# Kernel optimization log

Measured on AMD Instinct MI355X. Metric: run time of the kernel, lower is better.

## Reference

```python
import jax, jax.numpy as jnp
import numpy as np
from jax import lax

D_MODEL = 1024
D_STATE = 16
D_CONV = 4
EXPAND = 2
D_INNER = EXPAND * D_MODEL            # 2048
DT_RANK = (D_MODEL + 15) // 16        # 64
B, L = 2, 2048
EPS = 1e-5


def setup_inputs() -> dict:
    key = jax.random.key(0)
    ks = jax.random.split(key, 12)
    s = 0.02
    x = jax.random.normal(ks[0], (B, L, D_MODEL), dtype=jnp.float32)
    norm_w = jnp.ones((D_MODEL,), dtype=jnp.float32)
    in_proj_w = jax.random.normal(ks[1], (2 * D_INNER, D_MODEL), dtype=jnp.float32) * s
    conv_w = jax.random.normal(ks[2], (D_INNER, D_CONV), dtype=jnp.float32) * 0.1
    conv_b = jax.random.normal(ks[3], (D_INNER,), dtype=jnp.float32) * 0.01
    x_proj_w = jax.random.normal(ks[4], (DT_RANK + 2 * D_STATE, D_INNER), dtype=jnp.float32) * s
    dt_proj_w = jax.random.normal(ks[5], (D_INNER, DT_RANK), dtype=jnp.float32) * 0.1
    dt_proj_b = jax.random.normal(ks[6], (D_INNER,), dtype=jnp.float32) * 0.5 - 4.0  # small softplus(delta)
    # S4D-real init: A = -(1..d_state) per channel
    A_log = jnp.log(jnp.broadcast_to(jnp.arange(1, D_STATE + 1, dtype=jnp.float32), (D_INNER, D_STATE)))
    Dp = jnp.ones((D_INNER,), dtype=jnp.float32)
    out_proj_w = jax.random.normal(ks[7], (D_MODEL, D_INNER), dtype=jnp.float32) * s
    return {"x": x, "norm_w": norm_w, "in_proj_w": in_proj_w, "conv_w": conv_w,
            "conv_b": conv_b, "x_proj_w": x_proj_w, "dt_proj_w": dt_proj_w,
            "dt_proj_b": dt_proj_b, "A_log": A_log, "Dp": Dp, "out_proj_w": out_proj_w}


def _selective_scan(deltaA, deltaBu, Cm):
    # deltaA, deltaBu: [B,L,Di,N]; Cm: [B,L,N] -> y: [B,L,Di]
    def step(h, inp):
        dA, dBu, c = inp
        h = dA * h + dBu                       # [B,Di,N]
        y = jnp.einsum('bdn,bn->bd', h, c)     # [B,Di]
        return h, y
    h0 = jnp.zeros(deltaA.shape[0:1] + deltaA.shape[2:], deltaA.dtype)
    _, ys = lax.scan(step, h0, (deltaA.transpose(1, 0, 2, 3),
                                deltaBu.transpose(1, 0, 2, 3),
                                Cm.transpose(1, 0, 2)))
    return ys.transpose(1, 0, 2)               # [B,L,Di]


def reference(x, norm_w, in_proj_w, conv_w, conv_b, x_proj_w,
              dt_proj_w, dt_proj_b, A_log, Dp, out_proj_w):
    d_inner, d_conv = conv_w.shape
    d_state = A_log.shape[1]
    dt_rank = dt_proj_w.shape[1]

    # RMSNorm
    rms = jnp.sqrt(jnp.mean(x * x, axis=-1, keepdims=True) + EPS)
    xn = norm_w * (x / rms)

    # input projection -> x, z streams
    xz = jnp.einsum('bld,ed->ble', xn, in_proj_w)      # [B,L,2*Di]
    xi, z = jnp.split(xz, 2, axis=-1)

    # depthwise causal conv1d + SiLU
    xc = lax.conv_general_dilated(
        xi.transpose(0, 2, 1), conv_w[:, None, :], (1,), [(d_conv - 1, 0)],
        dimension_numbers=('NCL', 'OIL', 'NCL'), feature_group_count=d_inner)
    xc = jax.nn.silu(xc.transpose(0, 2, 1) + conv_b)   # [B,L,Di]

    # input-dependent SSM params
    dbl = jnp.einsum('bld,ed->ble', xc, x_proj_w)      # [B,L,dt_rank+2N]
    dt, Bm, Cm = jnp.split(dbl, [dt_rank, dt_rank + d_state], axis=-1)
    delta = jax.nn.softplus(jnp.einsum('blr,dr->bld', dt, dt_proj_w) + dt_proj_b)

    A = -jnp.exp(A_log)                                # [Di,N]
    deltaA = jnp.exp(delta[..., None] * A)             # [B,L,Di,N]
    deltaBu = delta[..., None] * Bm[:, :, None, :] * xc[..., None]

    y = _selective_scan(deltaA, deltaBu, Cm)           # [B,L,Di]
    y = y + xc * Dp
    y = y * jax.nn.silu(z)

    out = jnp.einsum('bld,ed->ble', y, out_proj_w)     # [B,L,d_model]
    return x + out
```

## Files before the change

kernel.cpp:

```cpp
#include <hip/hip_runtime.h>
#include <hip/hip_bf16.h>
#include <math.h>

#define D_MODEL 1024
#define D_STATE 16
#define D_CONV 4
#define D_INNER 2048
#define DT_RANK 64
#define BATCH 2
#define SEQ 2048
#define NTOK (BATCH*SEQ)
#define EPS 1e-5f
#define CCH 32
#define TCH (SEQ/CCH)
#define XKS 8
#define XKC (D_INNER/XKS)

typedef __attribute__((ext_vector_type(8))) short short8;
typedef __attribute__((ext_vector_type(4))) float f32x4;
typedef __attribute__((ext_vector_type(4))) unsigned short us4;

__device__ inline unsigned short f2bf(float f) {
  union { __hip_bfloat16 h; unsigned short u; } c;
  c.h = __float2bfloat16(f);
  return c.u;
}

#define GLL(gp, lp) __builtin_amdgcn_global_load_lds( \
    (const __attribute__((address_space(1))) void*)(gp), \
    (__attribute__((address_space(3))) void*)(lp), 16, 0, 0)

__global__ __launch_bounds__(256) void f2bf_kernel(const float* __restrict__ in,
                                                   unsigned short* __restrict__ out, int n) {
  int i = (blockIdx.x * 256 + threadIdx.x) * 4;
  if (i >= n) return;
  float4 v = *(const float4*)(in + i);
  us4 o;
  o[0] = f2bf(v.x); o[1] = f2bf(v.y); o[2] = f2bf(v.z); o[3] = f2bf(v.w);
  *(us4*)(out + i) = o;
}

__global__ __launch_bounds__(256) void rmsnorm_kernel(const float* __restrict__ x,
                                                      const float* __restrict__ w,
                                                      unsigned short* __restrict__ xn) {
  int tok = blockIdx.x;
  const float* xr = x + (size_t)tok * D_MODEL;
  unsigned short* xo = xn + (size_t)tok * D_MODEL;
  int t = threadIdx.x;
  float4 v = ((const float4*)xr)[t];
  float ss = v.x*v.x + v.y*v.y + v.z*v.z + v.w*v.w;
  #pragma unroll
  for (int off = 32; off > 0; off >>= 1) ss += __shfl_down(ss, off, 64);
  __shared__ float wsum[4];
  __shared__ float rinv_s;
  int lane = t & 63, wv = t >> 6;
  if (lane == 0) wsum[wv] = ss;
  __syncthreads();
  if (t == 0) {
    float tot = wsum[0] + wsum[1] + wsum[2] + wsum[3];
    rinv_s = 1.0f / sqrtf(tot / (float)D_MODEL + EPS);
  }
  __syncthreads();
  float rinv = rinv_s;
  float4 g = ((const float4*)w)[t];
  us4 o;
  o[0] = f2bf(v.x * rinv * g.x);
  o[1] = f2bf(v.y * rinv * g.y);
  o[2] = f2bf(v.z * rinv * g.z);
  o[3] = f2bf(v.w * rinv * g.w);
  *(us4*)(xo + t*4) = o;
}

template<int EPI>
__global__ __launch_bounds__(256) void gemm_bf16_kernel(
    const unsigned short* __restrict__ A,
    const unsigned short* __restrict__ W,
    float* __restrict__ C, int ldc, int K,
    const float* __restrict__ bias,
    const float* __restrict__ resid)
{
  __shared__ __align__(16) unsigned short Abuf[8*64*8];
  __shared__ __align__(16) unsigned short Bbuf[8*64*8];
  int tid = threadIdx.x;
  int lane = tid & 63;
  int w = tid >> 6;
  int bm = blockIdx.x * 128;
  int bn = blockIdx.y * 128;
  int wrow = (w >> 1) * 64;
  int wcol = (w & 1) * 64;

  int r15 = lane & 15, g = lane >> 4;
  const unsigned short* Ag0 = A + (size_t)(bm + 2*w*16 + r15) * K + g*8;
  const unsigned short* Ag1 = Ag0 + (size_t)16 * K;
  const unsigned short* Wg0 = W + (size_t)(bn + 2*w*16 + r15) * K + g*8;
  const unsigned short* Wg1 = Wg0 + (size_t)16 * K;
  unsigned short* Al0 = &Abuf[(2*w  )*512];
  unsigned short* Al1 = &Abuf[(2*w+1)*512];
  unsigned short* Bl0 = &Bbuf[(2*w  )*512];
  unsigned short* Bl1 = &Bbuf[(2*w+1)*512];

  f32x4 acc[4][4] = {};

  for (int k0 = 0; k0 < K; k0 += 32) {
    __syncthreads();
    GLL(Ag0 + k0, Al0);
    GLL(Ag1 + k0, Al1);
    GLL(Wg0 + k0, Bl0);
    GLL(Wg1 + k0, Bl1);
    __syncthreads();

    short8 af[4], bfr[4];
    #pragma unroll
    for (int i = 0; i < 4; ++i)
      af[i] = *(const short8*)&Abuf[((wrow >> 4) + i)*512 + lane*8];
    #pragma unroll
    for (int j = 0; j < 4; ++j)
      bfr[j] = *(const short8*)&Bbuf[((wcol >> 4) + j)*512 + lane*8];
    #pragma unroll
    for (int i = 0; i < 4; ++i)
      #pragma unroll
      for (int j = 0; j < 4; ++j)
        acc[i][j] = __builtin_amdgcn_mfma_f32_16x16x32_bf16(af[i], bfr[j], acc[i][j], 0, 0, 0);
  }

  #pragma unroll
  for (int i = 0; i < 4; ++i) {
    #pragma unroll
    for (int j = 0; j < 4; ++j) {
      #pragma unroll
      for (int r = 0; r < 4; ++r) {
        int row = bm + wrow + i*16 + (lane >> 4)*4 + r;
        int col = bn + wcol + j*16 + (lane & 15);
        float v = acc[i][j][r];
        if (EPI == 1) {
          float s = v + bias[col];
          v = fmaxf(s, 0.f) + log1pf(__expf(-fabsf(s)));
        } else if (EPI == 2) {
          v += resid[(size_t)row * ldc + col];
        }
        C[(size_t)row * ldc + col] = v;
      }
    }
  }
}

__global__ __launch_bounds__(256) void xproj_bf16_kernel(
    const unsigned short* __restrict__ A,
    const unsigned short* __restrict__ W,
    float* __restrict__ Ppart)
{
  __shared__ __align__(16) unsigned short Abuf[8*512];
  __shared__ __align__(16) unsigned short Bbuf[6*512];
  int tid = threadIdx.x;
  int lane = tid & 63;
  int w = tid >> 6;
  int bm = blockIdx.x * 128;
  int kc = blockIdx.y;
  const int K = D_INNER;
  int r15 = lane & 15, g = lane >> 4;

  const unsigned short* Ag0 = A + (size_t)(bm + 2*w*16 + r15) * K + g*8 + kc*XKC;
  const unsigned short* Ag1 = Ag0 + (size_t)16 * K;
  const unsigned short* Wg0 = W + (size_t)(w*16 + r15) * K + g*8 + kc*XKC;
  const unsigned short* Wg1 = W + (size_t)((4+w)*16 + r15) * K + g*8 + kc*XKC;
  unsigned short* Al0 = &Abuf[(2*w  )*512];
  unsigned short* Al1 = &Abuf[(2*w+1)*512];
  unsigned short* Bl0 = &Bbuf[w*512];
  unsigned short* Bl1 = &Bbuf[(4+w)*512];

  f32x4 acc[2][6] = {};

  for (int k0 = 0; k0 < XKC; k0 += 32) {
    __syncthreads();
    GLL(Ag0 + k0, Al0);
    GLL(Ag1 + k0, Al1);
    GLL(Wg0 + k0, Bl0);
    if (w < 2) GLL(Wg1 + k0, Bl1);
    __syncthreads();

    short8 af[2], bfr[6];
    #pragma unroll
    for (int i = 0; i < 2; ++i)
      af[i] = *(const short8*)&Abuf[(2*w + i)*512 + lane*8];
    #pragma unroll
    for (int j = 0; j < 6; ++j)
      bfr[j] = *(const short8*)&Bbuf[j*512 + lane*8];
    #pragma unroll
    for (int i = 0; i < 2; ++i)
      #pragma unroll
      for (int j = 0; j < 6; ++j)
        acc[i][j] = __builtin_amdgcn_mfma_f32_16x16x32_bf16(af[i], bfr[j], acc[i][j], 0, 0, 0);
  }

  float* out = Ppart + (size_t)kc * NTOK * 96;
  #pragma unroll
  for (int i = 0; i < 2; ++i) {
    #pragma unroll
    for (int j = 0; j < 6; ++j) {
      #pragma unroll
      for (int r = 0; r < 4; ++r) {
        int row = bm + w*32 + i*16 + (lane >> 4)*4 + r;
        int col = j*16 + (lane & 15);
        out[(size_t)row * 96 + col] = acc[i][j][r];
      }
    }
  }
}

__global__ __launch_bounds__(256) void xproj_reduce_kernel(
    const float* __restrict__ Ppart, float* __restrict__ dbl,
    unsigned short* __restrict__ dtbf)
{
  int idx = blockIdx.x * 256 + threadIdx.x;
  float s = 0.f;
  #pragma unroll
  for (int k = 0; k < XKS; ++k) s += Ppart[(size_t)k * NTOK * 96 + idx];
  dbl[idx] = s;
  int row = idx / 96, col = idx - row * 96;
  if (col < DT_RANK) dtbf[(size_t)row * DT_RANK + col] = f2bf(s);
}

__global__ __launch_bounds__(256) void conv_silu_kernel(
    const float* __restrict__ xz, const float* __restrict__ cw,
    const float* __restrict__ cb, float* __restrict__ xc,
    unsigned short* __restrict__ xcbf)
{
  int idx = blockIdx.x * 256 + threadIdx.x;
  int d = idx & (D_INNER - 1);
  int tok = idx >> 11;
  int l = tok & (SEQ - 1);
  float w0 = cw[d*4+0], w1 = cw[d*4+1], w2 = cw[d*4+2], w3 = cw[d*4+3];
  const float* xi = xz + (size_t)tok * (2*D_INNER) + d;
  float s = cb[d];
  s += (l >= 3 ? xi[-3*(2*D_INNER)] : 0.f) * w0;
  s += (l >= 2 ? xi[-2*(2*D_INNER)] : 0.f) * w1;
  s += (l >= 1 ? xi[-1*(2*D_INNER)] : 0.f) * w2;
  s += xi[0] * w3;
  float v = s / (1.f + __expf(-s));
  xc[idx] = v;
  xcbf[idx] = f2bf(v);
}

__global__ __launch_bounds__(256) void scan_pass1(
    const float* __restrict__ delta, const float* __restrict__ dbl,
    const float* __restrict__ xc, const float* __restrict__ A_log,
    float* __restrict__ P, float* __restrict__ He)
{
  int blk = blockIdx.x;
  int d = (blk & 7) * 256 + threadIdx.x;
  int c = (blk >> 3) & (CCH - 1);
  int b = blk >> 8;
  float Adn[16];
  #pragma unroll
  for (int n = 0; n < 16; ++n) Adn[n] = -__expf(A_log[d*16 + n]);
  float h[16] = {};
  float sdl = 0.f;
  int tok0 = b * SEQ + c * TCH;
  for (int t = 0; t < TCH; ++t) {
    size_t tok = (size_t)(tok0 + t);
    float dl = delta[tok * D_INNER + d];
    float xcv = xc[tok * D_INNER + d];
    float u = dl * xcv;
    const float4* bp = (const float4*)(dbl + tok*96 + 64);
    float4 b0 = bp[0], b1 = bp[1], b2 = bp[2], b3 = bp[3];
    float bv[16] = {b0.x,b0.y,b0.z,b0.w, b1.x,b1.y,b1.z,b1.w,
                    b2.x,b2.y,b2.z,b2.w, b3.x,b3.y,b3.z,b3.w};
    sdl += dl;
    #pragma unroll
    for (int n = 0; n < 16; ++n)
      h[n] = fmaf(__expf(dl * Adn[n]), h[n], u * bv[n]);
  }
  size_t base = ((size_t)(b*CCH + c) * 16) * D_INNER + d;
  #pragma unroll
  for (int n = 0; n < 16; ++n) {
    P [base + (size_t)n * D_INNER] = __expf(Adn[n] * sdl);
    He[base + (size_t)n * D_INNER] = h[n];
  }
}

__global__ __launch_bounds__(256) void scan_pass2(
    const float* __restrict__ P, const float* __restrict__ He,
    float* __restrict__ Hin)
{
  int blk = blockIdx.x;
  int d = (blk & 7) * 256 + threadIdx.x;
  int n = (blk >> 3) & 15;
  int b = blk >> 7;
  float h = 0.f;
  #pragma unroll 4
  for (int c = 0; c < CCH; ++c) {
    size_t idx = ((size_t)(b*CCH + c) * 16 + n) * D_INNER + d;
    Hin[idx] = h;
    h = fmaf(P[idx], h, He[idx]);
  }
}

__global__ __launch_bounds__(256) void scan_pass3(
    const float* __restrict__ delta, const float* __restrict__ dbl,
    const float* __restrict__ xc, const float* __restrict__ xz,
    const float* __restrict__ A_log, const float* __restrict__ Dp,
    const float* __restrict__ Hin, unsigned short* __restrict__ y)
{
  int blk = blockIdx.x;
  int d = (blk & 7) * 256 + threadIdx.x;
  int c = (blk >> 3) & (CCH - 1);
  int b = blk >> 8;
  float Adn[16];
  #pragma unroll
  for (int n = 0; n < 16; ++n) Adn[n] = -__expf(A_log[d*16 + n]);
  float Dpd = Dp[d];
  float h[16];
  size_t base = ((size_t)(b*CCH + c) * 16) * D_INNER + d;
  #pragma unroll
  for (int n = 0; n < 16; ++n) h[n] = Hin[base + (size_t)n * D_INNER];
  int tok0 = b * SEQ + c * TCH;
  for (int t = 0; t < TCH; ++t) {
    size_t tok = (size_t)(tok0 + t);
    float dl = delta[tok * D_INNER + d];
    float xcv = xc[tok * D_INNER + d];
    float u = dl * xcv;
    const float4* bp = (const float4*)(dbl + tok*96 + 64);
    float4 b0 = bp[0], b1 = bp[1], b2 = bp[2], b3 = bp[3];
    float4 c0 = bp[4], c1 = bp[5], c2 = bp[6], c3 = bp[7];
    float bv[16] = {b0.x,b0.y,b0.z,b0.w, b1.x,b1.y,b1.z,b1.w,
                    b2.x,b2.y,b2.z,b2.w, b3.x,b3.y,b3.z,b3.w};
    float cv[16] = {c0.x,c0.y,c0.z,c0.w, c1.x,c1.y,c1.z,c1.w,
                    c2.x,c2.y,c2.z,c2.w, c3.x,c3.y,c3.z,c3.w};
    float z = xz[tok * (2*D_INNER) + D_INNER + d];
    float acc = xcv * Dpd;
    #pragma unroll
    for (int n = 0; n < 16; ++n) {
      h[n] = fmaf(__expf(dl * Adn[n]), h[n], u * bv[n]);
      acc = fmaf(h[n], cv[n], acc);
    }
    float sz = z / (1.f + __expf(-z));
    y[tok * D_INNER + d] = f2bf(acc * sz);
  }
}

extern "C" void kernel_launch(void* const* d_in, const int* in_sizes, int n_in,
                              void* d_out, int out_size, void* d_ws, size_t ws_size,
                              hipStream_t stream) {
  const float* x         = (const float*)d_in[0];
  const float* norm_w    = (const float*)d_in[1];
  const float* in_proj_w = (const float*)d_in[2];
  const float* conv_w    = (const float*)d_in[3];
  const float* conv_b    = (const float*)d_in[4];
  const float* x_proj_w  = (const float*)d_in[5];
  const float* dt_proj_w = (const float*)d_in[6];
  const float* dt_proj_b = (const float*)d_in[7];
  const float* A_log     = (const float*)d_in[8];
  const float* Dp        = (const float*)d_in[9];
  const float* out_proj_w= (const float*)d_in[10];
  float* out = (float*)d_out;

  char* ws = (char*)d_ws;
  float*          xz      = (float*)(ws);
  float*          xc      = (float*)(ws + ( 64ull<<20));
  float*          dbl     = (float*)(ws + ( 96ull<<20));
  float*          delta   = (float*)(ws + ( 98ull<<20));
  unsigned short* xcbf    = (unsigned short*)(ws + ( 98ull<<20));
  unsigned short* xn_bf   = (unsigned short*)(ws + (130ull<<20));
  unsigned short* w_in_bf = (unsigned short*)(ws + (138ull<<20));
  float*          Ppart   = (float*)(ws + (130ull<<20));
  unsigned short* dtbf    = (unsigned short*)(ws + (144ull<<20));
  unsigned short* w_out_bf= (unsigned short*)(ws + (146ull<<20));
  unsigned short* yb_bf   = (unsigned short*)(ws + (150ull<<20));
  float*          Pst     = (float*)(ws + (130ull<<20));
  float*          Hest    = (float*)(ws + (138ull<<20));
  float*          Hin     = (float*)(ws + (166ull<<20));
  unsigned short* w_xp_bf = (unsigned short*)(ws + (166ull<<20));
  unsigned short* w_dt_bf = (unsigned short*)(ws + (167ull<<20));

  rmsnorm_kernel<<<NTOK, 256, 0, stream>>>(x, norm_w, xn_bf);

  f2bf_kernel<<<(2*D_INNER*D_MODEL)/1024, 256, 0, stream>>>(in_proj_w, w_in_bf, 2*D_INNER*D_MODEL);
  f2bf_kernel<<<(D_MODEL*D_INNER)/1024, 256, 0, stream>>>(out_proj_w, w_out_bf, D_MODEL*D_INNER);
  f2bf_kernel<<<(96*D_INNER)/1024, 256, 0, stream>>>(x_proj_w, w_xp_bf, 96*D_INNER);
  f2bf_kernel<<<(D_INNER*DT_RANK)/1024, 256, 0, stream>>>(dt_proj_w, w_dt_bf, D_INNER*DT_RANK);

  {
    dim3 g(NTOK/128, (2*D_INNER)/128);
    gemm_bf16_kernel<0><<<g, 256, 0, stream>>>(xn_bf, w_in_bf, xz, 2*D_INNER, D_MODEL,
                                               nullptr, nullptr);
  }

  conv_silu_kernel<<<(NTOK*D_INNER)/256, 256, 0, stream>>>(xz, conv_w, conv_b, xc, xcbf);

  {
    dim3 g(NTOK/128, XKS);
    xproj_bf16_kernel<<<g, 256, 0, stream>>>(xcbf, w_xp_bf, Ppart);
    xproj_reduce_kernel<<<(NTOK*96)/256, 256, 0, stream>>>(Ppart, dbl, dtbf);
  }

  {
    dim3 g(NTOK/128, D_INNER/128);
    gemm_bf16_kernel<1><<<g, 256, 0, stream>>>(dtbf, w_dt_bf, delta, D_INNER, DT_RANK,
                                               dt_proj_b, nullptr);
  }

  scan_pass1<<<BATCH*CCH*8, 256, 0, stream>>>(delta, dbl, xc, A_log, Pst, Hest);
  scan_pass2<<<BATCH*16*8, 256, 0, stream>>>(Pst, Hest, Hin);
  scan_pass3<<<BATCH*CCH*8, 256, 0, stream>>>(delta, dbl, xc, xz, A_log, Dp, Hin, yb_bf);

  {
    dim3 g(NTOK/128, D_MODEL/128);
    gemm_bf16_kernel<2><<<g, 256, 0, stream>>>(yb_bf, w_out_bf, out, D_MODEL, D_INNER,
                                               nullptr, x);
  }
}
```

Baseline: 390.0 us.

## Store intermediate activations in bf16 and merge weight conversion launches

The in_proj GEMM now writes xz in bf16 and the dt_proj GEMM writes delta in bf16. The conv kernel reads bf16 four channels at a time and writes only a bf16 xc, and the scan passes read these bf16 buffers. This roughly halves the memory traffic for the large intermediates, drops the fp32 xc copy, and folds the four weight-conversion launches into one. The trade-off is lower precision for delta, xc and z going into the recurrent scan, which could push results past the tolerance.

```diff
diff --git a/kernel.cpp b/kernel.cpp
--- a/kernel.cpp
+++ b/kernel.cpp
@@ -25,15 +25,29 @@
   c.h = __float2bfloat16(f);
   return c.u;
 }
+__device__ inline float bf2f(unsigned short u) {
+  union { unsigned int i; float f; } c;
+  c.i = ((unsigned int)u) << 16;
+  return c.f;
+}
 
 #define GLL(gp, lp) __builtin_amdgcn_global_load_lds( \
     (const __attribute__((address_space(1))) void*)(gp), \
     (__attribute__((address_space(3))) void*)(lp), 16, 0, 0)
 
-__global__ __launch_bounds__(256) void f2bf_kernel(const float* __restrict__ in,
-                                                   unsigned short* __restrict__ out, int n) {
-  int i = (blockIdx.x * 256 + threadIdx.x) * 4;
-  if (i >= n) return;
+__global__ __launch_bounds__(256) void f2bf4_kernel(
+    const float* __restrict__ i0, unsigned short* __restrict__ o0, int b0,
+    const float* __restrict__ i1, unsigned short* __restrict__ o1, int b1,
+    const float* __restrict__ i2, unsigned short* __restrict__ o2, int b2,
+    const float* __restrict__ i3, unsigned short* __restrict__ o3)
+{
+  int blk = blockIdx.x;
+  const float* in; unsigned short* out; int base;
+  if (blk < b0)           { in = i0; out = o0; base = blk; }
+  else if (blk < b0+b1)   { in = i1; out = o1; base = blk - b0; }
+  else if (blk < b0+b1+b2){ in = i2; out = o2; base = blk - b0 - b1; }
+  else                    { in = i3; out = o3; base = blk - b0 - b1 - b2; }
+  int i = (base*256 + threadIdx.x)*4;
   float4 v = *(const float4*)(in + i);
   us4 o;
   o[0] = f2bf(v.x); o[1] = f2bf(v.y); o[2] = f2bf(v.z); o[3] = f2bf(v.w);
@@ -71,11 +85,11 @@
   *(us4*)(xo + t*4) = o;
 }
 
-template<int EPI>
+template<int EPI, int OBF>
 __global__ __launch_bounds__(256) void gemm_bf16_kernel(
     const unsigned short* __restrict__ A,
     const unsigned short* __restrict__ W,
-    float* __restrict__ C, int ldc, int K,
+    void* __restrict__ Cv, int ldc, int K,
     const float* __restrict__ bias,
     const float* __restrict__ resid)
 {
@@ -138,7 +152,8 @@
         } else if (EPI == 2) {
           v += resid[(size_t)row * ldc + col];
         }
-        C[(size_t)row * ldc + col] = v;
+        if (OBF) ((unsigned short*)Cv)[(size_t)row * ldc + col] = f2bf(v);
+        else     ((float*)Cv)[(size_t)row * ldc + col] = v;
       }
     }
   }
@@ -221,29 +236,39 @@
 }
 
 __global__ __launch_bounds__(256) void conv_silu_kernel(
-    const float* __restrict__ xz, const float* __restrict__ cw,
-    const float* __restrict__ cb, float* __restrict__ xc,
-    unsigned short* __restrict__ xcbf)
+    const unsigned short* __restrict__ xz, const float* __restrict__ cw,
+    const float* __restrict__ cb, unsigned short* __restrict__ xcbf)
 {
   int idx = blockIdx.x * 256 + threadIdx.x;
-  int d = idx & (D_INNER - 1);
-  int tok = idx >> 11;
+  int dq = idx & (D_INNER/4 - 1);
+  int tok = idx >> 9;
   int l = tok & (SEQ - 1);
-  float w0 = cw[d*4+0], w1 = cw[d*4+1], w2 = cw[d*4+2], w3 = cw[d*4+3];
-  const float* xi = xz + (size_t)tok * (2*D_INNER) + d;
-  float s = cb[d];
-  s += (l >= 3 ? xi[-3*(2*D_INNER)] : 0.f) * w0;
-  s += (l >= 2 ? xi[-2*(2*D_INNER)] : 0.f) * w1;
-  s += (l >= 1 ? xi[-1*(2*D_INNER)] : 0.f) * w2;
-  s += xi[0] * w3;
-  float v = s / (1.f + __expf(-s));
-  xc[idx] = v;
-  xcbf[idx] = f2bf(v);
+  int d = dq * 4;
+  const unsigned short* xi = xz + (size_t)tok * (2*D_INNER) + d;
+  us4 v3 = *(const us4*)xi;
+  us4 v2 = l >= 1 ? *(const us4*)(xi - 1*(2*D_INNER)) : (us4)0;
+  us4 v1 = l >= 2 ? *(const us4*)(xi - 2*(2*D_INNER)) : (us4)0;
+  us4 v0 = l >= 3 ? *(const us4*)(xi - 3*(2*D_INNER)) : (us4)0;
+  float4 cbv = *(const float4*)(cb + d);
+  float cbx[4] = {cbv.x, cbv.y, cbv.z, cbv.w};
+  us4 o;
+  #pragma unroll
+  for (int j = 0; j < 4; ++j) {
+    float4 wv = *(const float4*)(cw + (d + j) * 4);
+    float s = cbx[j];
+    s = fmaf(bf2f(v0[j]), wv.x, s);
+    s = fmaf(bf2f(v1[j]), wv.y, s);
+    s = fmaf(bf2f(v2[j]), wv.z, s);
+    s = fmaf(bf2f(v3[j]), wv.w, s);
+    float v = s / (1.f + __expf(-s));
+    o[j] = f2bf(v);
+  }
+  *(us4*)(xcbf + (size_t)tok * D_INNER + d) = o;
 }
 
 __global__ __launch_bounds__(256) void scan_pass1(
-    const float* __restrict__ delta, const float* __restrict__ dbl,
-    const float* __restrict__ xc, const float* __restrict__ A_log,
+    const unsigned short* __restrict__ delta, const float* __restrict__ dbl,
+    const unsigned short* __restrict__ xc, const float* __restrict__ A_log,
     float* __restrict__ P, float* __restrict__ He)
 {
   int blk = blockIdx.x;
@@ -258,8 +283,8 @@
   int tok0 = b * SEQ + c * TCH;
   for (int t = 0; t < TCH; ++t) {
     size_t tok = (size_t)(tok0 + t);
-    float dl = delta[tok * D_INNER + d];
-    float xcv = xc[tok * D_INNER + d];
+    float dl = bf2f(delta[tok * D_INNER + d]);
+    float xcv = bf2f(xc[tok * D_INNER + d]);
     float u = dl * xcv;
     const float4* bp = (const float4*)(dbl + tok*96 + 64);
     float4 b0 = bp[0], b1 = bp[1], b2 = bp[2], b3 = bp[3];
@@ -296,8 +321,8 @@
 }
 
 __global__ __launch_bounds__(256) void scan_pass3(
-    const float* __restrict__ delta, const float* __restrict__ dbl,
-    const float* __restrict__ xc, const float* __restrict__ xz,
+    const unsigned short* __restrict__ delta, const float* __restrict__ dbl,
+    const unsigned short* __restrict__ xc, const unsigned short* __restrict__ xz,
     const float* __restrict__ A_log, const float* __restrict__ Dp,
     const float* __restrict__ Hin, unsigned short* __restrict__ y)
 {
@@ -316,8 +341,8 @@
   int tok0 = b * SEQ + c * TCH;
   for (int t = 0; t < TCH; ++t) {
     size_t tok = (size_t)(tok0 + t);
-    float dl = delta[tok * D_INNER + d];
-    float xcv = xc[tok * D_INNER + d];
+    float dl = bf2f(delta[tok * D_INNER + d]);
+    float xcv = bf2f(xc[tok * D_INNER + d]);
     float u = dl * xcv;
     const float4* bp = (const float4*)(dbl + tok*96 + 64);
     float4 b0 = bp[0], b1 = bp[1], b2 = bp[2], b3 = bp[3];
@@ -326,7 +351,7 @@
                     b2.x,b2.y,b2.z,b2.w, b3.x,b3.y,b3.z,b3.w};
     float cv[16] = {c0.x,c0.y,c0.z,c0.w, c1.x,c1.y,c1.z,c1.w,
                     c2.x,c2.y,c2.z,c2.w, c3.x,c3.y,c3.z,c3.w};
-    float z = xz[tok * (2*D_INNER) + D_INNER + d];
+    float z = bf2f(xz[tok * (2*D_INNER) + D_INNER + d]);
     float acc = xcv * Dpd;
     #pragma unroll
     for (int n = 0; n < 16; ++n) {
@@ -355,57 +380,57 @@
   float* out = (float*)d_out;
 
   char* ws = (char*)d_ws;
-  float*          xz      = (float*)(ws);
-  float*          xc      = (float*)(ws + ( 64ull<<20));
-  float*          dbl     = (float*)(ws + ( 96ull<<20));
-  float*          delta   = (float*)(ws + ( 98ull<<20));
-  unsigned short* xcbf    = (unsigned short*)(ws + ( 98ull<<20));
-  unsigned short* xn_bf   = (unsigned short*)(ws + (130ull<<20));
-  unsigned short* w_in_bf = (unsigned short*)(ws + (138ull<<20));
-  float*          Ppart   = (float*)(ws + (130ull<<20));
-  unsigned short* dtbf    = (unsigned short*)(ws + (144ull<<20));
-  unsigned short* w_out_bf= (unsigned short*)(ws + (146ull<<20));
-  unsigned short* yb_bf   = (unsigned short*)(ws + (150ull<<20));
-  float*          Pst     = (float*)(ws + (130ull<<20));
-  float*          Hest    = (float*)(ws + (138ull<<20));
-  float*          Hin     = (float*)(ws + (166ull<<20));
-  unsigned short* w_xp_bf = (unsigned short*)(ws + (166ull<<20));
-  unsigned short* w_dt_bf = (unsigned short*)(ws + (167ull<<20));
+  unsigned short* xz_bf   = (unsigned short*)(ws);
+  unsigned short* xc_bf   = (unsigned short*)(ws + ( 32ull<<20));
+  float*          dbl     = (float*)(ws + ( 48ull<<20));
+  unsigned short* delta_bf= (unsigned short*)(ws + ( 50ull<<20));
+  unsigned short* xn_bf   = (unsigned short*)(ws + ( 66ull<<20));
+  unsigned short* w_in_bf = (unsigned short*)(ws + ( 74ull<<20));
+  unsigned short* w_out_bf= (unsigned short*)(ws + ( 82ull<<20));
+  unsigned short* w_xp_bf = (unsigned short*)(ws + ( 86ull<<20));
+  unsigned short* w_dt_bf = (unsigned short*)(ws + ( 87ull<<20));
+  unsigned short* dtbf    = (unsigned short*)(ws + ( 88ull<<20));
+  float*          Ppart   = (float*)(ws + ( 89ull<<20));
+  float*          Pst     = (float*)(ws + (102ull<<20));
+  float*          Hest    = (float*)(ws + (110ull<<20));
+  float*          Hin     = (float*)(ws + (118ull<<20));
+  unsigned short* yb_bf   = (unsigned short*)(ws + (126ull<<20));
 
   rmsnorm_kernel<<<NTOK, 256, 0, stream>>>(x, norm_w, xn_bf);
 
-  f2bf_kernel<<<(2*D_INNER*D_MODEL)/1024, 256, 0, stream>>>(in_proj_w, w_in_bf, 2*D_INNER*D_MODEL);
-  f2bf_kernel<<<(D_MODEL*D_INNER)/1024, 256, 0, stream>>>(out_proj_w, w_out_bf, D_MODEL*D_INNER);
-  f2bf_kernel<<<(96*D_INNER)/1024, 256, 0, stream>>>(x_proj_w, w_xp_bf, 96*D_INNER);
-  f2bf_kernel<<<(D_INNER*DT_RANK)/1024, 256, 0, stream>>>(dt_proj_w, w_dt_bf, D_INNER*DT_RANK);
+  f2bf4_kernel<<<4096+2048+192+128, 256, 0, stream>>>(
+      in_proj_w, w_in_bf, 4096,
+      out_proj_w, w_out_bf, 2048,
+      x_proj_w, w_xp_bf, 192,
+      dt_proj_w, w_dt_bf);
 
   {
     dim3 g(NTOK/128, (2*D_INNER)/128);
-    gemm_bf16_kernel<0><<<g, 256, 0, stream>>>(xn_bf, w_in_bf, xz, 2*D_INNER, D_MODEL,
-                                               nullptr, nullptr);
-  }
-
-  conv_silu_kernel<<<(NTOK*D_INNER)/256, 256, 0, stream>>>(xz, conv_w, conv_b, xc, xcbf);
+    gemm_bf16_kernel<0,1><<<g, 256, 0, stream>>>(xn_bf, w_in_bf, xz_bf, 2*D_INNER, D_MODEL,
+                                                 nullptr, nullptr);
+  }
+
+  conv_silu_kernel<<<(NTOK*D_INNER/4)/256, 256, 0, stream>>>(xz_bf, conv_w, conv_b, xc_bf);
 
   {
     dim3 g(NTOK/128, XKS);
-    xproj_bf16_kernel<<<g, 256, 0, stream>>>(xcbf, w_xp_bf, Ppart);
+    xproj_bf16_kernel<<<g, 256, 0, stream>>>(xc_bf, w_xp_bf, Ppart);
     xproj_reduce_kernel<<<(NTOK*96)/256, 256, 0, stream>>>(Ppart, dbl, dtbf);
   }
 
   {
     dim3 g(NTOK/128, D_INNER/128);
-    gemm_bf16_kernel<1><<<g, 256, 0, stream>>>(dtbf, w_dt_bf, delta, D_INNER, DT_RANK,
-                                               dt_proj_b, nullptr);
-  }
-
-  scan_pass1<<<BATCH*CCH*8, 256, 0, stream>>>(delta, dbl, xc, A_log, Pst, Hest);
+    gemm_bf16_kernel<1,1><<<g, 256, 0, stream>>>(dtbf, w_dt_bf, delta_bf, D_INNER, DT_RANK,
+                                                 dt_proj_b, nullptr);
+  }
+
+  scan_pass1<<<BATCH*CCH*8, 256, 0, stream>>>(delta_bf, dbl, xc_bf, A_log, Pst, Hest);
   scan_pass2<<<BATCH*16*8, 256, 0, stream>>>(Pst, Hest, Hin);
-  scan_pass3<<<BATCH*CCH*8, 256, 0, stream>>>(delta, dbl, xc, xz, A_log, Dp, Hin, yb_bf);
+  scan_pass3<<<BATCH*CCH*8, 256, 0, stream>>>(delta_bf, dbl, xc_bf, xz_bf, A_log, Dp, Hin, yb_bf);
 
   {
     dim3 g(NTOK/128, D_MODEL/128);
-    gemm_bf16_kernel<2><<<g, 256, 0, stream>>>(yb_bf, w_out_bf, out, D_MODEL, D_INNER,
-                                               nullptr, x);
-  }
-}
+    gemm_bf16_kernel<2,0><<<g, 256, 0, stream>>>(yb_bf, w_out_bf, out, D_MODEL, D_INNER,
+                                                 nullptr, x);
+  }
+}
```

After: 385.3 us. Within noise of the previous version (-1.2%).
